# Performance work log

Hardware: AMD Instinct MI355X
Metric: run time of the kernel (lower is better)

## Reference

```python
import jax, jax.numpy as jnp
import numpy as np

B, S, D = 1, 4096, 512      # batch, seq, model dim
E, K, H = 64, 2, 256        # routed experts, top-k, expert hidden (moe_inter_dim)
HS = 2048                   # shared expert hidden = n_shared_experts * inter_dim
EPS = 1e-5                  # LayerNorm eps (torch default)


def setup_inputs() -> dict:
    key = jax.random.key(0)
    ks = jax.random.split(key, 16)
    n = lambda k, shp, s=0.02: jax.random.normal(k, shp, dtype=jnp.float32) * s
    return {
        "x": jax.random.normal(ks[0], (B, S, D), dtype=jnp.float32),
        # gate Linear(dim -> E)
        "Wg": n(ks[1], (E, D)), "bg": n(ks[2], (E,)),
        # per-expert LayerNorm affine
        "gamma": 1.0 + n(ks[3], (E, D)), "beta": n(ks[4], (E, D)),
        # per-expert SwiGLU: w1, w3: D->H ; w2: H->D
        "W1": n(ks[5], (E, D, H)), "b1": n(ks[6], (E, H)),
        "W3": n(ks[7], (E, D, H)), "b3": n(ks[8], (E, H)),
        "W2": n(ks[9], (E, H, D)), "b2": n(ks[10], (E, D)),
        # shared expert (same Expert structure, hidden HS)
        "gs": 1.0 + n(ks[11], (D,)), "bs": n(ks[11], (D,)),
        "Ws1": n(ks[12], (D, HS)), "bs1": n(ks[12], (HS,)),
        "Ws3": n(ks[13], (D, HS)), "bs3": n(ks[13], (HS,)),
        "Ws2": n(ks[14], (HS, D)), "bs2": n(ks[15], (D,)),
    }


def reference(x, Wg, bg, gamma, beta, W1, b1, W3, b3, W2, b2,
              gs, bs, Ws1, bs1, Ws3, bs3, Ws2, bs2):
    shape = x.shape
    xt = x.reshape(-1, D)                      # [T, D] tokens
    T = xt.shape[0]

    # ---- Gate (eval path: sigmoid scores, no load balancing / bias / groups) ----
    scores = jax.nn.sigmoid(xt @ Wg.T + bg)    # [T, E]
    w, idx = jax.lax.top_k(scores, K)          # [T, K]
    w = w / w.sum(-1, keepdims=True)           # sigmoid path normalization; route_scale = 1
    # dense combine weights: cw[t, e] = routing weight of token t on expert e (0 if not routed)
    cw = jnp.zeros((T, E), xt.dtype).at[jnp.arange(T)[:, None], idx].add(w)

    # ---- Shared LayerNorm statistics (affine folded per-expert below) ----
    mu = xt.mean(-1, keepdims=True)
    var = ((xt - mu) ** 2).mean(-1, keepdims=True)
    nx = (xt - mu) * jax.lax.rsqrt(var + EPS)  # [T, D], unit-affine normalized

    # Fold each expert's LN affine (gamma_e, beta_e) into its w1/w3:
    # (nx*g + b) @ W = nx @ (g[:,None]*W) + b @ W
    W1p = gamma[:, :, None] * W1
    b1p = b1 + jnp.einsum('ed,edh->eh', beta, W1)
    W3p = gamma[:, :, None] * W3
    b3p = b3 + jnp.einsum('ed,edh->eh', beta, W3)

    h1 = jnp.einsum('td,edh->eth', nx, W1p) + b1p[:, None, :]   # [E, T, H]
    h3 = jnp.einsum('td,edh->eth', nx, W3p) + b3p[:, None, :]
    h = jax.nn.silu(h1) * h3                                     # SwiGLU, [E, T, H]

    # Weighted combine: y[t] = sum_e cw[t,e] * (h[e,t] @ W2[e] + b2[e])
    hw = h * cw.T[:, :, None]                                    # [E, T, H]
    y = jnp.einsum('eth,ehd->td', hw, W2) + cw @ b2              # [T, D]

    # ---- Shared expert (applied to every token) ----
    nxs = nx * gs + bs
    hs = jax.nn.silu(nxs @ Ws1 + bs1) * (nxs @ Ws3 + bs3)        # [T, HS]
    z = hs @ Ws2 + bs2

    return (y + z).reshape(shape)
```

## Files before the change

### kernel.cpp

```cpp
#include <hip/hip_runtime.h>
#include <math.h>

typedef unsigned short u16;
typedef __attribute__((ext_vector_type(8))) short bf16x8;
typedef __attribute__((ext_vector_type(4))) float f32x4;

#define TT   4096
#define DM   512
#define NE   64
#define HE   256
#define HSH  2048
#define NSH  8
#define PADBASE 16384
#define MAXTILES 384
#define MAXRT    128

#define WAITV(N) asm volatile("s_waitcnt vmcnt(" #N ")" ::: "memory")
#define SBAR()   __builtin_amdgcn_s_barrier()
#define SCHEDB() __builtin_amdgcn_sched_barrier(0)

__device__ __forceinline__ float sig_(float z){ return 1.f/(1.f+__expf(-z)); }

__device__ __forceinline__ u16 f2bf(float x){
  unsigned int u = __builtin_bit_cast(unsigned int, x);
  u = (u + 0x7FFFu + ((u >> 16) & 1u)) >> 16;
  return (u16)u;
}

__device__ __forceinline__ f32x4 mfma16(bf16x8 a, bf16x8 b, f32x4 c){
  return __builtin_amdgcn_mfma_f32_16x16x32_bf16(a, b, c, 0, 0, 0);
}

__device__ __forceinline__ bf16x8 frd(const char* tile, int row, int csw){
  return *(const bf16x8*)(tile + row*64 + csw);
}

__device__ __forceinline__ void gl16(const void* g, void* l){
  __builtin_amdgcn_global_load_lds(
      (const __attribute__((address_space(1))) unsigned int*)g,
      (__attribute__((address_space(3))) unsigned int*)l, 16, 0, 0);
}

struct CvtJob {
  const float* in; const float* scale; const float* fvec;
  u16* out; float* fout; int K; int N; int base;
};
struct CvtJobs { CvtJob j[6]; };

__global__ __launch_bounds__(256) void k_cvt_all(CvtJobs jobs)
{
  const int bid = blockIdx.x;
  int ji = 0;
  #pragma unroll
  for (int i = 1; i < 6; i++) ji = (bid >= jobs.j[i].base) ? i : ji;
  const CvtJob J = jobs.j[ji];
  const int local = bid - J.base;
  const int nbx = J.K >> 6, nby = J.N >> 6;
  const int pm = nbx * nby;
  const int z = local / pm, rem = local - z*pm;
  const int bx = rem % nbx, by = rem / nbx;

  __shared__ u16 T[64][80];
  __shared__ float red[64][65];
  const int tid = threadIdx.x;
  const int k0 = bx*64, n0 = by*64;
  const float* ip = J.in + (size_t)z * J.K * J.N;
  const int r = tid>>2, cb = (tid&3)*16;
  const float sc = J.scale ? J.scale[(size_t)z*J.K + k0 + r] : 1.0f;
  const float fv = J.fvec  ? J.fvec [(size_t)z*J.K + k0 + r] : 0.0f;
  #pragma unroll
  for (int jj = 0; jj < 4; jj++){
    float4 v = *(const float4*)(ip + (size_t)(k0+r)*J.N + n0 + cb + jj*4);
    T[cb+jj*4+0][r] = f2bf(v.x*sc);
    T[cb+jj*4+1][r] = f2bf(v.y*sc);
    T[cb+jj*4+2][r] = f2bf(v.z*sc);
    T[cb+jj*4+3][r] = f2bf(v.w*sc);
    if (J.fout){
      red[cb+jj*4+0][r] = v.x*fv;
      red[cb+jj*4+1][r] = v.y*fv;
      red[cb+jj*4+2][r] = v.z*fv;
      red[cb+jj*4+3][r] = v.w*fv;
    }
  }
  __syncthreads();
  if (J.fout){
    const int c = tid & 63, rq = tid >> 6;
    float s = 0.f;
    #pragma unroll
    for (int rr = 0; rr < 16; rr++) s += red[c][rq*16 + rr];
    atomicAdd(J.fout + (size_t)z*J.N + n0 + c, s);
  }
  const int n = tid>>2, kb = (tid&3)*16;
  uint4 a = *(const uint4*)&T[n][kb];
  uint4 b = *(const uint4*)&T[n][kb+8];
  u16* op = J.out + (size_t)z*J.K*J.N;
  *(uint4*)(op + (size_t)(n0+n)*J.K + k0 + kb)     = a;
  *(uint4*)(op + (size_t)(n0+n)*J.K + k0 + kb + 8) = b;
}

__global__ __launch_bounds__(256) void k_ln_gate(
    const float* __restrict__ x, const float* __restrict__ Wg, const float* __restrict__ bg,
    u16* __restrict__ nxb, int* __restrict__ top_idx, float* __restrict__ top_w)
{
  __shared__ float xs[DM];
  __shared__ float sred[4], ssred[4];
  __shared__ float sc[NE];
  const int tid = threadIdx.x;
  const int t   = blockIdx.x;

  float2 v = reinterpret_cast<const float2*>(x + (size_t)t*DM)[tid];
  xs[2*tid]   = v.x;
  xs[2*tid+1] = v.y;
  float s  = v.x + v.y;
  float ss = v.x*v.x + v.y*v.y;
  #pragma unroll
  for (int o = 32; o > 0; o >>= 1){ s += __shfl_xor(s, o); ss += __shfl_xor(ss, o); }
  const int wid = tid >> 6, lane = tid & 63;
  if (lane == 0){ sred[wid] = s; ssred[wid] = ss; }
  __syncthreads();
  const float tot = sred[0]+sred[1]+sred[2]+sred[3];
  const float tss = ssred[0]+ssred[1]+ssred[2]+ssred[3];
  const float mu  = tot * (1.f/DM);
  const float var = tss * (1.f/DM) - mu*mu;
  const float rstd = rsqrtf(var + 1e-5f);
  unsigned int pk = (unsigned int)f2bf((v.x-mu)*rstd) | ((unsigned int)f2bf((v.y-mu)*rstd) << 16);
  *(unsigned int*)(nxb + (size_t)t*DM + 2*tid) = pk;

  const int e = tid >> 2, sub = tid & 3;
  const float4* wrow4 = reinterpret_cast<const float4*>(Wg + (size_t)e*DM);
  const float4* xs4   = reinterpret_cast<const float4*>(xs);
  float acc = 0.f;
  #pragma unroll 4
  for (int i = sub; i < DM/4; i += 4){
    const float4 w = wrow4[i]; const float4 xv = xs4[i];
    acc += xv.x*w.x + xv.y*w.y + xv.z*w.z + xv.w*w.w;
  }
  acc += __shfl_xor(acc, 1);
  acc += __shfl_xor(acc, 2);
  if (sub == 0) sc[e] = acc + bg[e];
  __syncthreads();

  if (tid < 64) {
    const float s0 = sc[tid];
    float m = s0; int mi = tid;
    #pragma unroll
    for (int o = 1; o < 64; o <<= 1){
      float om = __shfl_xor(m, o); int oi = __shfl_xor(mi, o);
      if (om > m || (om == m && oi < mi)) { m = om; mi = oi; }
    }
    float s1 = (tid == mi) ? -INFINITY : s0;
    float m2 = s1; int mi2 = tid;
    #pragma unroll
    for (int o = 1; o < 64; o <<= 1){
      float om = __shfl_xor(m2, o); int oi = __shfl_xor(mi2, o);
      if (om > m2 || (om == m2 && oi < mi2)) { m2 = om; mi2 = oi; }
    }
    if (tid == 0){
      const float w0 = sig_(m), w1 = sig_(m2);
      const float inv = 1.f/(w0+w1);
      top_idx[2*t]   = mi;
      top_idx[2*t+1] = mi2;
      top_w[2*t]     = w0*inv;
      top_w[2*t+1]   = w1*inv;
    }
  }
}

__global__ __launch_bounds__(256) void k_route(
    const int* __restrict__ top_idx, const float* __restrict__ top_w,
    int* __restrict__ bucket_tok, float* __restrict__ bucket_w,
    int* __restrict__ tiles, int* __restrict__ n_tiles)
{
  __shared__ int cnt[NE], base_[NE];
  __shared__ int nroute;
  const int tid = threadIdx.x;
  if (tid < NE) cnt[tid] = 0;
  __syncthreads();
  for (int p = tid; p < TT*2; p += 256) atomicAdd(&cnt[top_idx[p]], 1);
  __syncthreads();
  if (tid == 0){
    int run = 0, ntl = 0;
    for (int e = 0; e < NE; e++){
      base_[e] = run;
      const int c = cnt[e];
      for (int b = 0; b < c; b += 128){
        const int n = (c - b < 128) ? (c - b) : 128;
        tiles[ntl++] = (e << 17) | (((run + b) >> 7) << 8) | n;
      }
      run += ((c + 127) >> 7) << 7;
    }
    nroute = ntl;
    n_tiles[0] = ntl + NSH*(TT/128);
    n_tiles[1] = ntl;
  }
  __syncthreads();
  if (tid < NSH*(TT/128)){
    const int s = tid >> 5, t = tid & 31;
    const int b0 = PADBASE + s*TT + t*128;
    tiles[nroute + tid] = ((NE + s) << 17) | ((b0 >> 7) << 8) | 128;
  }
  if (tid < NE) cnt[tid] = 0;
  __syncthreads();
  for (int p = tid; p < TT*2; p += 256){
    const int e = top_idx[p];
    const int pos = base_[e] + atomicAdd(&cnt[e], 1);
    bucket_tok[pos] = p >> 1;
    bucket_w[pos]   = top_w[p];
  }
}

__global__ __launch_bounds__(512) void k_up(
    const u16* __restrict__ nxb,
    const u16* __restrict__ W1bT, const u16* __restrict__ W3bT,
    const u16* __restrict__ Ws1bT, const u16* __restrict__ Ws3bT,
    const float* __restrict__ b1, const float* __restrict__ b3,
    const float* __restrict__ bs1, const float* __restrict__ bs3,
    const float* __restrict__ b1f, const float* __restrict__ b3f,
    const int* __restrict__ bucket_tok, const float* __restrict__ bucket_w,
    const int* __restrict__ tiles, const int* __restrict__ n_tiles,
    u16* __restrict__ hrout, u16* __restrict__ hs)
{
  if ((int)blockIdx.x >= n_tiles[0]) return;
  const int info = tiles[blockIdx.x];
  const int e  = info >> 17;
  const int b0 = ((info >> 8) & 0x1FF) << 7;
  const int nt = info & 255;
  const bool sh = (e >= NE);
  const int y  = blockIdx.y;

  __shared__ __align__(16) char Ab[3][8192];
  __shared__ __align__(16) char B1b[3][8192];
  __shared__ __align__(16) char B3b[3][8192];
  __shared__ int   toks[128];
  __shared__ float tw[128];

  const int tid = threadIdx.x, wid = tid >> 6, lane = tid & 63;
  const int l15 = lane & 15, q = lane >> 4;

  if (tid < 128){
    int tk; float w;
    if (!sh){
      if (tid < nt){ tk = bucket_tok[b0+tid]; w = bucket_w[b0+tid]; }
      else         { tk = 0; w = 0.f; }
    } else {
      tk = ((b0 - PADBASE) & (TT-1)) + tid; w = 1.f;
    }
    toks[tid] = tk; tw[tid] = w;
  }
  __syncthreads();

  const u16* w1e = sh ? (Ws1bT + (size_t)(e-NE)*HE*DM) : (W1bT + (size_t)e*HE*DM);
  const u16* w3e = sh ? (Ws3bT + (size_t)(e-NE)*HE*DM) : (W3bT + (size_t)e*HE*DM);

  const int srow = lane >> 2;
  const int csrc = (((lane & 3) ^ ((lane >> 3) & 3))) * 8;
  const u16* asrc = nxb + (size_t)toks[wid*16 + srow]*DM + csrc;
  const u16* b1s  = w1e + (size_t)(y*128 + wid*16 + srow)*DM + csrc;
  const u16* b3s  = w3e + (size_t)(y*128 + wid*16 + srow)*DM + csrc;
  const int loff = wid*1024;

#define UP_STAGE(ph, k0) do{ \
    gl16(asrc + (k0), Ab[ph] + loff); \
    gl16(b1s  + (k0), B1b[ph] + loff); \
    gl16(b3s  + (k0), B3b[ph] + loff); \
  } while(0)

  const int wm = (wid & 1)*64, wn = (wid >> 1)*32;

  const float* ob1 = sh ? (bs1 + (size_t)(e-NE)*HE) : (b1 + (size_t)e*HE);
  const float* ob3 = sh ? (bs3 + (size_t)(e-NE)*HE) : (b3 + (size_t)e*HE);
  f32x4 acc1[4][2], acc3[4][2];
  #pragma unroll
  for (int fn = 0; fn < 2; fn++){
    const int h = y*128 + wn + fn*16 + l15;
    const float v1 = ob1[h] + b1f[(size_t)e*HE + h];
    const float v3 = ob3[h] + b3f[(size_t)e*HE + h];
    #pragma unroll
    for (int fm = 0; fm < 4; fm++){
      acc1[fm][fn] = (f32x4){v1,v1,v1,v1};
      acc3[fm][fn] = (f32x4){v3,v3,v3,v3};
    }
  }

  UP_STAGE(0, 0);
  UP_STAGE(1, 32);
  const int csw = (q ^ ((l15 >> 1) & 3)) * 16;

  for (int ks = 0; ks < DM/32; ks++){
    const int cur = ks % 3;
    if (ks + 2 < DM/32) UP_STAGE((ks+2)%3, (ks+2)*32);
    if (ks < DM/32 - 2)       WAITV(6);
    else if (ks == DM/32 - 2) WAITV(3);
    else                      WAITV(0);
    SBAR();
    __builtin_amdgcn_s_setprio(1);
    const char* A  = Ab[cur];
    const char* B1 = B1b[cur];
    const char* B3 = B3b[cur];
    bf16x8 fa[4];
    #pragma unroll
    for (int fm = 0; fm < 4; fm++) fa[fm] = frd(A, wm + fm*16 + l15, csw);
    #pragma unroll
    for (int fn = 0; fn < 2; fn++){
      bf16x8 fb1 = frd(B1, wn + fn*16 + l15, csw);
      bf16x8 fb3 = frd(B3, wn + fn*16 + l15, csw);
      #pragma unroll
      for (int fm = 0; fm < 4; fm++){
        acc1[fm][fn] = mfma16(fa[fm], fb1, acc1[fm][fn]);
        acc3[fm][fn] = mfma16(fa[fm], fb3, acc3[fm][fn]);
      }
    }
    __builtin_amdgcn_s_setprio(0);
    SCHEDB();
    SBAR();
  }
#undef UP_STAGE

  const int tbase = sh ? ((b0 - PADBASE) & (TT-1)) : 0;
  const int scol  = sh ? (e - NE)*HE : 0;
  #pragma unroll
  for (int fm = 0; fm < 4; fm++){
    #pragma unroll
    for (int fn = 0; fn < 2; fn++){
      const int hl = y*128 + wn + fn*16 + l15;
      #pragma unroll
      for (int r = 0; r < 4; r++){
        const int m = wm + fm*16 + 4*q + r;
        float v = 0.f;
        if (m < nt){
          const float a1 = acc1[fm][fn][r];
          const float a3 = acc3[fm][fn][r];
          v = a1 * sig_(a1) * a3 * tw[m];
        }
        if (sh) hs[(size_t)(tbase+m)*HSH + scol + hl] = f2bf(v);
        else    hrout[(size_t)(b0+m)*HE + hl] = f2bf(v);
      }
    }
  }
}

__global__ __launch_bounds__(256) void k_down_shared(
    const u16* __restrict__ hs, const u16* __restrict__ Ws2bT,
    const float* __restrict__ bs2, float* __restrict__ out)
{
  __shared__ __align__(16) char Ab[3][4096];
  __shared__ __align__(16) char Bb[3][8192];

  const int tid = threadIdx.x, wid = tid >> 6, lane = tid & 63;
  const int l15 = lane & 15, q = lane >> 4;
  const int t0 = blockIdx.x*64, d0 = blockIdx.y*128;

  const int srow = tid >> 2;
  const int csrc = (((tid & 3) ^ ((tid >> 3) & 3))) * 8;
  const u16* asrc  = hs    + (size_t)(t0 + srow)*HSH + csrc;
  const u16* bsrc0 = Ws2bT + (size_t)(d0 + srow)*HSH + csrc;
  const u16* bsrc1 = Ws2bT + (size_t)(d0 + 64 + srow)*HSH + csrc;
  const int loff = wid*1024;

#define DS_STAGE(ph, k0) do{ \
    gl16(asrc  + (k0), Ab[ph] + loff); \
    gl16(bsrc0 + (k0), Bb[ph] + loff); \
    gl16(bsrc1 + (k0), Bb[ph] + 4096 + loff); \
  } while(0)

  const int wm = (wid & 1)*32, wn = (wid >> 1)*64;

  f32x4 acc[2][4];
  #pragma unroll
  for (int fm = 0; fm < 2; fm++)
    #pragma unroll
    for (int fn = 0; fn < 4; fn++) acc[fm][fn] = (f32x4){0.f,0.f,0.f,0.f};

  DS_STAGE(0, 0);
  DS_STAGE(1, 32);
  const int csw = (q ^ ((l15 >> 1) & 3)) * 16;

  for (int ks = 0; ks < HSH/32; ks++){
    const int cur = ks % 3;
    if (ks + 2 < HSH/32) DS_STAGE((ks+2)%3, (ks+2)*32);
    if (ks < HSH/32 - 2)       WAITV(6);
    else if (ks == HSH/32 - 2) WAITV(3);
    else                       WAITV(0);
    SBAR();
    __builtin_amdgcn_s_setprio(1);
    const char* A = Ab[cur];
    const char* B = Bb[cur];
    bf16x8 fa[2];
    #pragma unroll
    for (int fm = 0; fm < 2; fm++) fa[fm] = frd(A, wm + fm*16 + l15, csw);
    #pragma unroll
    for (int fn = 0; fn < 4; fn++){
      bf16x8 fb = frd(B, wn + fn*16 + l15, csw);
      #pragma unroll
      for (int fm = 0; fm < 2; fm++)
        acc[fm][fn] = mfma16(fa[fm], fb, acc[fm][fn]);
    }
    __builtin_amdgcn_s_setprio(0);
    SCHEDB();
    SBAR();
  }
#undef DS_STAGE

  #pragma unroll
  for (int fm = 0; fm < 2; fm++){
    #pragma unroll
    for (int fn = 0; fn < 4; fn++){
      const int d = d0 + wn + fn*16 + l15;
      const float bv = bs2[d];
      #pragma unroll
      for (int r = 0; r < 4; r++){
        const int t = t0 + wm + fm*16 + 4*q + r;
        out[(size_t)t*DM + d] = acc[fm][fn][r] + bv;
      }
    }
  }
}

__global__ __launch_bounds__(512) void k_down_routed(
    const u16* __restrict__ hrout, const u16* __restrict__ W2bT,
    const float* __restrict__ b2,
    const int* __restrict__ bucket_tok, const float* __restrict__ bucket_w,
    const int* __restrict__ tiles, const int* __restrict__ n_tiles,
    float* __restrict__ out)
{
  if ((int)blockIdx.x >= n_tiles[1]) return;
  const int info = tiles[blockIdx.x];
  const int e  = info >> 17;
  const int b0 = ((info >> 8) & 0x1FF) << 7;
  const int nt = info & 255;
  const int d0 = blockIdx.y * 256;

  __shared__ __align__(16) char Ab[3][8192];
  __shared__ __align__(16) char Bb[3][16384];
  __shared__ int   toks[128];
  __shared__ float tw[128];

  const int tid = threadIdx.x, wid = tid >> 6, lane = tid & 63;
  const int l15 = lane & 15, q = lane >> 4;

  if (tid < 128){
    if (tid < nt){ toks[tid] = bucket_tok[b0+tid]; tw[tid] = bucket_w[b0+tid]; }
    else         { toks[tid] = 0; tw[tid] = 0.f; }
  }
  __syncthreads();

  const u16* w2e = W2bT + (size_t)e*DM*HE;
  const int srow = tid >> 2;
  const int csrc = (((tid & 3) ^ ((tid >> 3) & 3))) * 8;
  const u16* asrc  = hrout + (size_t)(b0 + srow)*HE + csrc;
  const u16* bsrc0 = w2e + (size_t)(d0 + srow)*HE + csrc;
  const u16* bsrc1 = w2e + (size_t)(d0 + 128 + srow)*HE + csrc;
  const int loff = wid*1024;

#define DR_STAGE(ph, k0) do{ \
    gl16(asrc  + (k0), Ab[ph] + loff); \
    gl16(bsrc0 + (k0), Bb[ph] + loff); \
    gl16(bsrc1 + (k0), Bb[ph] + 8192 + loff); \
  } while(0)

  const int wm = (wid & 1)*64, wn = (wid >> 1)*64;

  f32x4 acc[4][4];
  #pragma unroll
  for (int fm = 0; fm < 4; fm++)
    #pragma unroll
    for (int fn = 0; fn < 4; fn++) acc[fm][fn] = (f32x4){0.f,0.f,0.f,0.f};

  DR_STAGE(0, 0);
  DR_STAGE(1, 32);
  const int csw = (q ^ ((l15 >> 1) & 3)) * 16;

  for (int ks = 0; ks < HE/32; ks++){
    const int cur = ks % 3;
    if (ks + 2 < HE/32) DR_STAGE((ks+2)%3, (ks+2)*32);
    if (ks < HE/32 - 2)       WAITV(6);
    else if (ks == HE/32 - 2) WAITV(3);
    else                      WAITV(0);
    SBAR();
    __builtin_amdgcn_s_setprio(1);
    const char* A = Ab[cur];
    const char* B = Bb[cur];
    bf16x8 fa[4];
    #pragma unroll
    for (int fm = 0; fm < 4; fm++) fa[fm] = frd(A, wm + fm*16 + l15, csw);
    #pragma unroll
    for (int fn = 0; fn < 4; fn++){
      bf16x8 fb = frd(B, wn + fn*16 + l15, csw);
      #pragma unroll
      for (int fm = 0; fm < 4; fm++)
        acc[fm][fn] = mfma16(fa[fm], fb, acc[fm][fn]);
    }
    __builtin_amdgcn_s_setprio(0);
    SCHEDB();
    SBAR();
  }
#undef DR_STAGE

  #pragma unroll
  for (int fm = 0; fm < 4; fm++){
    #pragma unroll
    for (int fn = 0; fn < 4; fn++){
      const int d = d0 + wn + fn*16 + l15;
      #pragma unroll
      for (int r = 0; r < 4; r++){
        const int m = wm + fm*16 + 4*q + r;
        if (m < nt)
          atomicAdd(out + (size_t)toks[m]*DM + d, acc[fm][fn][r] + tw[m]*b2[(size_t)e*DM + d]);
      }
    }
  }
}

extern "C" void kernel_launch(void* const* d_in, const int* in_sizes, int n_in,
                              void* d_out, int out_size, void* d_ws, size_t ws_size,
                              hipStream_t stream)
{
  (void)in_sizes; (void)n_in; (void)ws_size; (void)out_size;
  const float* x     = (const float*)d_in[0];
  const float* Wg    = (const float*)d_in[1];
  const float* bg    = (const float*)d_in[2];
  const float* gamma = (const float*)d_in[3];
  const float* beta  = (const float*)d_in[4];
  const float* W1    = (const float*)d_in[5];
  const float* b1    = (const float*)d_in[6];
  const float* W3    = (const float*)d_in[7];
  const float* b3    = (const float*)d_in[8];
  const float* W2    = (const float*)d_in[9];
  const float* b2    = (const float*)d_in[10];
  const float* gs    = (const float*)d_in[11];
  const float* bs    = (const float*)d_in[12];
  const float* Ws1   = (const float*)d_in[13];
  const float* bs1   = (const float*)d_in[14];
  const float* Ws3   = (const float*)d_in[15];
  const float* bs3   = (const float*)d_in[16];
  const float* Ws2   = (const float*)d_in[17];
  const float* bs2   = (const float*)d_in[18];
  float* out = (float*)d_out;

  char* ws = (char*)d_ws;
  size_t off = 0;
  auto alloc = [&](size_t bytes) -> char* {
    char* p = ws + off;
    off += (bytes + 255) & ~(size_t)255;
    return p;
  };
  u16*   nxb        = (u16*)  alloc((size_t)TT*DM*2);
  int*   top_idx    = (int*)  alloc((size_t)TT*2*4);
  float* top_w      = (float*)alloc((size_t)TT*2*4);
  int*   bucket_tok = (int*)  alloc((size_t)PADBASE*4);
  float* bucket_w   = (float*)alloc((size_t)PADBASE*4);
  int*   tiles      = (int*)  alloc(MAXTILES*4);
  int*   n_tiles    = (int*)  alloc(64);
  u16*   hrout      = (u16*)  alloc((size_t)PADBASE*HE*2);
  u16*   hs         = (u16*)  alloc((size_t)TT*HSH*2);
  u16*   W1bT       = (u16*)  alloc((size_t)NE*HE*DM*2);
  u16*   W3bT       = (u16*)  alloc((size_t)NE*HE*DM*2);
  u16*   W2bT       = (u16*)  alloc((size_t)NE*DM*HE*2);
  u16*   Ws1bT      = (u16*)  alloc((size_t)HSH*DM*2);
  u16*   Ws3bT      = (u16*)  alloc((size_t)HSH*DM*2);
  u16*   Ws2bT      = (u16*)  alloc((size_t)DM*HSH*2);
  float* b1f        = (float*)alloc((size_t)(NE*HE + HSH)*4);
  float* b3f        = (float*)alloc((size_t)(NE*HE + HSH)*4);

  hipMemsetAsync(b1f, 0, (size_t)(NE*HE + HSH)*4, stream);
  hipMemsetAsync(b3f, 0, (size_t)(NE*HE + HSH)*4, stream);
  CvtJobs jobs;
  jobs.j[0] = { W1,  gamma, beta, W1bT,  b1f,          DM,  HE,  0    };
  jobs.j[1] = { W3,  gamma, beta, W3bT,  b3f,          DM,  HE,  2048 };
  jobs.j[2] = { W2,  nullptr, nullptr, W2bT, nullptr,  HE,  DM,  4096 };
  jobs.j[3] = { Ws1, gs, bs, Ws1bT, b1f + NE*HE,       DM,  HSH, 6144 };
  jobs.j[4] = { Ws3, gs, bs, Ws3bT, b3f + NE*HE,       DM,  HSH, 6400 };
  jobs.j[5] = { Ws2, nullptr, nullptr, Ws2bT, nullptr, HSH, DM,  6656 };
  k_cvt_all<<<dim3(6912), 256, 0, stream>>>(jobs);

  k_ln_gate<<<dim3(TT), 256, 0, stream>>>(x, Wg, bg, nxb, top_idx, top_w);
  k_route<<<dim3(1), 256, 0, stream>>>(top_idx, top_w, bucket_tok, bucket_w, tiles, n_tiles);

  k_up<<<dim3(MAXTILES, 2), 512, 0, stream>>>(nxb, W1bT, W3bT, Ws1bT, Ws3bT,
                                              b1, b3, bs1, bs3, b1f, b3f,
                                              bucket_tok, bucket_w, tiles, n_tiles, hrout, hs);
  k_down_shared<<<dim3(TT/64, DM/128), 256, 0, stream>>>(hs, Ws2bT, bs2, out);
  k_down_routed<<<dim3(MAXRT, 2), 512, 0, stream>>>(hrout, W2bT, b2,
                                                    bucket_tok, bucket_w, tiles, n_tiles, out);
}
```

Baseline: 204.9 us.

## Merge weight conversion with LN/gate and fuse shared and routed down kernels

```diff
diff --git a/kernel.cpp b/kernel.cpp
--- a/kernel.cpp
+++ b/kernel.cpp
@@ -2,6 +2,7 @@
 #include <math.h>
 
 typedef unsigned short u16;
+typedef unsigned int u32;
 typedef __attribute__((ext_vector_type(8))) short bf16x8;
 typedef __attribute__((ext_vector_type(4))) float f32x4;
 
@@ -22,7 +23,7 @@
 __device__ __forceinline__ float sig_(float z){ return 1.f/(1.f+__expf(-z)); }
 
 __device__ __forceinline__ u16 f2bf(float x){
-  unsigned int u = __builtin_bit_cast(unsigned int, x);
+  u32 u = __builtin_bit_cast(u32, x);
   u = (u + 0x7FFFu + ((u >> 16) & 1u)) >> 16;
   return (u16)u;
 }
@@ -47,66 +48,66 @@
 };
 struct CvtJobs { CvtJob j[6]; };
 
-__global__ __launch_bounds__(256) void k_cvt_all(CvtJobs jobs)
+__global__ __launch_bounds__(256) void k_pre(
+    CvtJobs jobs, int ln_base,
+    const float* __restrict__ x, const float* __restrict__ Wg,
+    const float* __restrict__ bg,
+    u16* __restrict__ nxb, int* __restrict__ top_idx, float* __restrict__ top_w)
 {
   const int bid = blockIdx.x;
-  int ji = 0;
-  #pragma unroll
-  for (int i = 1; i < 6; i++) ji = (bid >= jobs.j[i].base) ? i : ji;
-  const CvtJob J = jobs.j[ji];
-  const int local = bid - J.base;
-  const int nbx = J.K >> 6, nby = J.N >> 6;
-  const int pm = nbx * nby;
-  const int z = local / pm, rem = local - z*pm;
-  const int bx = rem % nbx, by = rem / nbx;
-
-  __shared__ u16 T[64][80];
-  __shared__ float red[64][65];
   const int tid = threadIdx.x;
-  const int k0 = bx*64, n0 = by*64;
-  const float* ip = J.in + (size_t)z * J.K * J.N;
-  const int r = tid>>2, cb = (tid&3)*16;
-  const float sc = J.scale ? J.scale[(size_t)z*J.K + k0 + r] : 1.0f;
-  const float fv = J.fvec  ? J.fvec [(size_t)z*J.K + k0 + r] : 0.0f;
-  #pragma unroll
-  for (int jj = 0; jj < 4; jj++){
-    float4 v = *(const float4*)(ip + (size_t)(k0+r)*J.N + n0 + cb + jj*4);
-    T[cb+jj*4+0][r] = f2bf(v.x*sc);
-    T[cb+jj*4+1][r] = f2bf(v.y*sc);
-    T[cb+jj*4+2][r] = f2bf(v.z*sc);
-    T[cb+jj*4+3][r] = f2bf(v.w*sc);
-    if (J.fout){
-      red[cb+jj*4+0][r] = v.x*fv;
-      red[cb+jj*4+1][r] = v.y*fv;
-      red[cb+jj*4+2][r] = v.z*fv;
-      red[cb+jj*4+3][r] = v.w*fv;
-    }
-  }
-  __syncthreads();
-  if (J.fout){
-    const int c = tid & 63, rq = tid >> 6;
-    float s = 0.f;
-    #pragma unroll
-    for (int rr = 0; rr < 16; rr++) s += red[c][rq*16 + rr];
-    atomicAdd(J.fout + (size_t)z*J.N + n0 + c, s);
-  }
-  const int n = tid>>2, kb = (tid&3)*16;
-  uint4 a = *(const uint4*)&T[n][kb];
-  uint4 b = *(const uint4*)&T[n][kb+8];
-  u16* op = J.out + (size_t)z*J.K*J.N;
-  *(uint4*)(op + (size_t)(n0+n)*J.K + k0 + kb)     = a;
-  *(uint4*)(op + (size_t)(n0+n)*J.K + k0 + kb + 8) = b;
-}
-
-__global__ __launch_bounds__(256) void k_ln_gate(
-    const float* __restrict__ x, const float* __restrict__ Wg, const float* __restrict__ bg,
-    u16* __restrict__ nxb, int* __restrict__ top_idx, float* __restrict__ top_w)
-{
+
+  if (bid < ln_base){
+    int ji = 0;
+    #pragma unroll
+    for (int i = 1; i < 6; i++) ji = (bid >= jobs.j[i].base) ? i : ji;
+    const CvtJob J = jobs.j[ji];
+    const int local = bid - J.base;
+    const int nbk = J.K >> 6;
+    const int nbn = J.N >> 8;
+    const int pm = nbk * nbn;
+    const int z = local / pm, rem = local - z*pm;
+    const int kt = rem % nbk, ntile = rem / nbk;
+    const int k0 = kt*64;
+    const int n  = ntile*256 + tid;
+
+    const float* src = J.in + (size_t)z*J.K*J.N + (size_t)k0*J.N + n;
+    const float* scp = J.scale ? (J.scale + (size_t)z*J.K + k0) : nullptr;
+    const float* fvp = J.fvec  ? (J.fvec  + (size_t)z*J.K + k0) : nullptr;
+    u16* dst = J.out + (size_t)z*J.K*J.N + (size_t)n*J.K + k0;
+
+    float fsum = 0.f;
+    for (int kk = 0; kk < 8; kk++){
+      float v[8];
+      #pragma unroll
+      for (int j = 0; j < 8; j++) v[j] = src[(size_t)(kk*8 + j)*J.N];
+      u16 b[8];
+      if (scp){
+        #pragma unroll
+        for (int j = 0; j < 8; j++) b[j] = f2bf(v[j]*scp[kk*8 + j]);
+      } else {
+        #pragma unroll
+        for (int j = 0; j < 8; j++) b[j] = f2bf(v[j]);
+      }
+      if (fvp){
+        #pragma unroll
+        for (int j = 0; j < 8; j++) fsum += v[j]*fvp[kk*8 + j];
+      }
+      uint4 pk;
+      pk.x = (u32)b[0] | ((u32)b[1] << 16);
+      pk.y = (u32)b[2] | ((u32)b[3] << 16);
+      pk.z = (u32)b[4] | ((u32)b[5] << 16);
+      pk.w = (u32)b[6] | ((u32)b[7] << 16);
+      *(uint4*)(dst + kk*8) = pk;
+    }
+    if (J.fout) atomicAdd(J.fout + (size_t)z*J.N + n, fsum);
+    return;
+  }
+
   __shared__ float xs[DM];
   __shared__ float sred[4], ssred[4];
   __shared__ float sc[NE];
-  const int tid = threadIdx.x;
-  const int t   = blockIdx.x;
+  const int t = bid - ln_base;
 
   float2 v = reinterpret_cast<const float2*>(x + (size_t)t*DM)[tid];
   xs[2*tid]   = v.x;
@@ -123,8 +124,8 @@
   const float mu  = tot * (1.f/DM);
   const float var = tss * (1.f/DM) - mu*mu;
   const float rstd = rsqrtf(var + 1e-5f);
-  unsigned int pk = (unsigned int)f2bf((v.x-mu)*rstd) | ((unsigned int)f2bf((v.y-mu)*rstd) << 16);
-  *(unsigned int*)(nxb + (size_t)t*DM + 2*tid) = pk;
+  u32 pk = (u32)f2bf((v.x-mu)*rstd) | ((u32)f2bf((v.y-mu)*rstd) << 16);
+  *(u32*)(nxb + (size_t)t*DM + 2*tid) = pk;
 
   const int e = tid >> 2, sub = tid & 3;
   const float4* wrow4 = reinterpret_cast<const float4*>(Wg + (size_t)e*DM);
@@ -339,104 +340,104 @@
   }
 }
 
-__global__ __launch_bounds__(256) void k_down_shared(
+__global__ __launch_bounds__(512) void k_down(
     const u16* __restrict__ hs, const u16* __restrict__ Ws2bT,
-    const float* __restrict__ bs2, float* __restrict__ out)
-{
-  __shared__ __align__(16) char Ab[3][4096];
-  __shared__ __align__(16) char Bb[3][8192];
-
-  const int tid = threadIdx.x, wid = tid >> 6, lane = tid & 63;
-  const int l15 = lane & 15, q = lane >> 4;
-  const int t0 = blockIdx.x*64, d0 = blockIdx.y*128;
-
-  const int srow = tid >> 2;
-  const int csrc = (((tid & 3) ^ ((tid >> 3) & 3))) * 8;
-  const u16* asrc  = hs    + (size_t)(t0 + srow)*HSH + csrc;
-  const u16* bsrc0 = Ws2bT + (size_t)(d0 + srow)*HSH + csrc;
-  const u16* bsrc1 = Ws2bT + (size_t)(d0 + 64 + srow)*HSH + csrc;
-  const int loff = wid*1024;
-
-#define DS_STAGE(ph, k0) do{ \
-    gl16(asrc  + (k0), Ab[ph] + loff); \
-    gl16(bsrc0 + (k0), Bb[ph] + loff); \
-    gl16(bsrc1 + (k0), Bb[ph] + 4096 + loff); \
-  } while(0)
-
-  const int wm = (wid & 1)*32, wn = (wid >> 1)*64;
-
-  f32x4 acc[2][4];
-  #pragma unroll
-  for (int fm = 0; fm < 2; fm++)
-    #pragma unroll
-    for (int fn = 0; fn < 4; fn++) acc[fm][fn] = (f32x4){0.f,0.f,0.f,0.f};
-
-  DS_STAGE(0, 0);
-  DS_STAGE(1, 32);
-  const int csw = (q ^ ((l15 >> 1) & 3)) * 16;
-
-  for (int ks = 0; ks < HSH/32; ks++){
-    const int cur = ks % 3;
-    if (ks + 2 < HSH/32) DS_STAGE((ks+2)%3, (ks+2)*32);
-    if (ks < HSH/32 - 2)       WAITV(6);
-    else if (ks == HSH/32 - 2) WAITV(3);
-    else                       WAITV(0);
-    SBAR();
-    __builtin_amdgcn_s_setprio(1);
-    const char* A = Ab[cur];
-    const char* B = Bb[cur];
-    bf16x8 fa[2];
-    #pragma unroll
-    for (int fm = 0; fm < 2; fm++) fa[fm] = frd(A, wm + fm*16 + l15, csw);
-    #pragma unroll
-    for (int fn = 0; fn < 4; fn++){
-      bf16x8 fb = frd(B, wn + fn*16 + l15, csw);
-      #pragma unroll
-      for (int fm = 0; fm < 2; fm++)
-        acc[fm][fn] = mfma16(fa[fm], fb, acc[fm][fn]);
-    }
-    __builtin_amdgcn_s_setprio(0);
-    SCHEDB();
-    SBAR();
-  }
-#undef DS_STAGE
-
-  #pragma unroll
-  for (int fm = 0; fm < 2; fm++){
-    #pragma unroll
-    for (int fn = 0; fn < 4; fn++){
-      const int d = d0 + wn + fn*16 + l15;
-      const float bv = bs2[d];
-      #pragma unroll
-      for (int r = 0; r < 4; r++){
-        const int t = t0 + wm + fm*16 + 4*q + r;
-        out[(size_t)t*DM + d] = acc[fm][fn][r] + bv;
-      }
-    }
-  }
-}
-
-__global__ __launch_bounds__(512) void k_down_routed(
+    const float* __restrict__ bs2,
     const u16* __restrict__ hrout, const u16* __restrict__ W2bT,
     const float* __restrict__ b2,
     const int* __restrict__ bucket_tok, const float* __restrict__ bucket_w,
     const int* __restrict__ tiles, const int* __restrict__ n_tiles,
     float* __restrict__ out)
 {
-  if ((int)blockIdx.x >= n_tiles[1]) return;
-  const int info = tiles[blockIdx.x];
+  __shared__ __align__(16) char LDS[73728];
+  __shared__ int   toks[128];
+  __shared__ float tw[128];
+
+  const int tid = threadIdx.x, wid = tid >> 6, lane = tid & 63;
+  const int l15 = lane & 15, q = lane >> 4;
+  const int csw  = (q ^ ((l15 >> 1) & 3)) * 16;
+  const int srow = tid >> 2;
+  const int csrc = ((tid & 3) ^ ((tid >> 3) & 3)) * 8;
+  const int loff = wid*1024;
+
+  if ((int)blockIdx.x < 128){
+    const int t0 = (blockIdx.x >> 2) * 128;
+    const int d0 = (blockIdx.x & 3) * 128;
+    char* Ab = LDS;
+    char* Bb = LDS + 24576;
+
+    const u16* asrc = hs    + (size_t)(t0 + srow)*HSH + csrc;
+    const u16* bsrc = Ws2bT + (size_t)(d0 + srow)*HSH + csrc;
+
+#define DS_STAGE(ph, k0) do{ \
+    gl16(asrc + (k0), Ab + (ph)*8192 + loff); \
+    gl16(bsrc + (k0), Bb + (ph)*8192 + loff); \
+  } while(0)
+
+    const int wm = (wid & 1)*64, wn = (wid >> 1)*32;
+
+    f32x4 acc[4][2];
+    #pragma unroll
+    for (int fm = 0; fm < 4; fm++)
+      #pragma unroll
+      for (int fn = 0; fn < 2; fn++) acc[fm][fn] = (f32x4){0.f,0.f,0.f,0.f};
+
+    DS_STAGE(0, 0);
+    DS_STAGE(1, 32);
+
+    for (int ks = 0; ks < HSH/32; ks++){
+      const int cur = ks % 3;
+      if (ks + 2 < HSH/32) DS_STAGE((ks+2)%3, (ks+2)*32);
+      if (ks < HSH/32 - 2)       WAITV(4);
+      else if (ks == HSH/32 - 2) WAITV(2);
+      else                       WAITV(0);
+      SBAR();
+      __builtin_amdgcn_s_setprio(1);
+      const char* A = Ab + cur*8192;
+      const char* B = Bb + cur*8192;
+      bf16x8 fa[4];
+      #pragma unroll
+      for (int fm = 0; fm < 4; fm++) fa[fm] = frd(A, wm + fm*16 + l15, csw);
+      #pragma unroll
+      for (int fn = 0; fn < 2; fn++){
+        bf16x8 fb = frd(B, wn + fn*16 + l15, csw);
+        #pragma unroll
+        for (int fm = 0; fm < 4; fm++)
+          acc[fm][fn] = mfma16(fa[fm], fb, acc[fm][fn]);
+      }
+      __builtin_amdgcn_s_setprio(0);
+      SCHEDB();
+      SBAR();
+    }
+#undef DS_STAGE
+
+    #pragma unroll
+    for (int fm = 0; fm < 4; fm++){
+      #pragma unroll
+      for (int fn = 0; fn < 2; fn++){
+        const int d = d0 + wn + fn*16 + l15;
+        const float bv = bs2[d];
+        #pragma unroll
+        for (int r = 0; r < 4; r++){
+          const int t = t0 + wm + fm*16 + 4*q + r;
+          atomicAdd(out + (size_t)t*DM + d, acc[fm][fn][r] + bv);
+        }
+      }
+    }
+    return;
+  }
+
+  const int rb = (int)blockIdx.x - 128;
+  const int ti = rb >> 1;
+  if (ti >= n_tiles[1]) return;
+  const int info = tiles[ti];
   const int e  = info >> 17;
   const int b0 = ((info >> 8) & 0x1FF) << 7;
   const int nt = info & 255;
-  const int d0 = blockIdx.y * 256;
-
-  __shared__ __align__(16) char Ab[3][8192];
-  __shared__ __align__(16) char Bb[3][16384];
-  __shared__ int   toks[128];
-  __shared__ float tw[128];
-
-  const int tid = threadIdx.x, wid = tid >> 6, lane = tid & 63;
-  const int l15 = lane & 15, q = lane >> 4;
+  const int d0 = (rb & 1) * 256;
+
+  char* Ab = LDS;
+  char* Bb = LDS + 24576;
 
   if (tid < 128){
     if (tid < nt){ toks[tid] = bucket_tok[b0+tid]; tw[tid] = bucket_w[b0+tid]; }
@@ -445,17 +446,14 @@
   __syncthreads();
 
   const u16* w2e = W2bT + (size_t)e*DM*HE;
-  const int srow = tid >> 2;
-  const int csrc = (((tid & 3) ^ ((tid >> 3) & 3))) * 8;
   const u16* asrc  = hrout + (size_t)(b0 + srow)*HE + csrc;
   const u16* bsrc0 = w2e + (size_t)(d0 + srow)*HE + csrc;
   const u16* bsrc1 = w2e + (size_t)(d0 + 128 + srow)*HE + csrc;
-  const int loff = wid*1024;
 
 #define DR_STAGE(ph, k0) do{ \
-    gl16(asrc  + (k0), Ab[ph] + loff); \
-    gl16(bsrc0 + (k0), Bb[ph] + loff); \
-    gl16(bsrc1 + (k0), Bb[ph] + 8192 + loff); \
+    gl16(asrc  + (k0), Ab + (ph)*8192  + loff); \
+    gl16(bsrc0 + (k0), Bb + (ph)*16384 + loff); \
+    gl16(bsrc1 + (k0), Bb + (ph)*16384 + 8192 + loff); \
   } while(0)
 
   const int wm = (wid & 1)*64, wn = (wid >> 1)*64;
@@ -468,7 +466,6 @@
 
   DR_STAGE(0, 0);
   DR_STAGE(1, 32);
-  const int csw = (q ^ ((l15 >> 1) & 3)) * 16;
 
   for (int ks = 0; ks < HE/32; ks++){
     const int cur = ks % 3;
@@ -478,8 +475,8 @@
     else                      WAITV(0);
     SBAR();
     __builtin_amdgcn_s_setprio(1);
-    const char* A = Ab[cur];
-    const char* B = Bb[cur];
+    const char* A = Ab + cur*8192;
+    const char* B = Bb + cur*16384;
     bf16x8 fa[4];
     #pragma unroll
     for (int fm = 0; fm < 4; fm++) fa[fm] = frd(A, wm + fm*16 + l15, csw);
@@ -515,7 +512,7 @@
                               void* d_out, int out_size, void* d_ws, size_t ws_size,
                               hipStream_t stream)
 {
-  (void)in_sizes; (void)n_in; (void)ws_size; (void)out_size;
+  (void)in_sizes; (void)n_in; (void)ws_size;
   const float* x     = (const float*)d_in[0];
   const float* Wg    = (const float*)d_in[1];
   const float* bg    = (const float*)d_in[2];
@@ -564,22 +561,24 @@
 
   hipMemsetAsync(b1f, 0, (size_t)(NE*HE + HSH)*4, stream);
   hipMemsetAsync(b3f, 0, (size_t)(NE*HE + HSH)*4, stream);
+  hipMemsetAsync(out, 0, (size_t)out_size*sizeof(float), stream);
+
   CvtJobs jobs;
-  jobs.j[0] = { W1,  gamma, beta, W1bT,  b1f,          DM,  HE,  0    };
-  jobs.j[1] = { W3,  gamma, beta, W3bT,  b3f,          DM,  HE,  2048 };
-  jobs.j[2] = { W2,  nullptr, nullptr, W2bT, nullptr,  HE,  DM,  4096 };
-  jobs.j[3] = { Ws1, gs, bs, Ws1bT, b1f + NE*HE,       DM,  HSH, 6144 };
-  jobs.j[4] = { Ws3, gs, bs, Ws3bT, b3f + NE*HE,       DM,  HSH, 6400 };
-  jobs.j[5] = { Ws2, nullptr, nullptr, Ws2bT, nullptr, HSH, DM,  6656 };
-  k_cvt_all<<<dim3(6912), 256, 0, stream>>>(jobs);
-
-  k_ln_gate<<<dim3(TT), 256, 0, stream>>>(x, Wg, bg, nxb, top_idx, top_w);
+  jobs.j[0] = { W1,  gamma,   beta,    W1bT,  b1f,          DM,  HE,  0    };
+  jobs.j[1] = { W3,  gamma,   beta,    W3bT,  b3f,          DM,  HE,  512  };
+  jobs.j[2] = { W2,  nullptr, nullptr, W2bT,  nullptr,      HE,  DM,  1024 };
+  jobs.j[3] = { Ws1, gs,      bs,      Ws1bT, b1f + NE*HE,  DM,  HSH, 1536 };
+  jobs.j[4] = { Ws3, gs,      bs,      Ws3bT, b3f + NE*HE,  DM,  HSH, 1600 };
+  jobs.j[5] = { Ws2, nullptr, nullptr, Ws2bT, nullptr,      HSH, DM,  1664 };
+  const int ln_base = 1728;
+  k_pre<<<dim3(ln_base + TT), 256, 0, stream>>>(jobs, ln_base,
+                                                x, Wg, bg, nxb, top_idx, top_w);
+
   k_route<<<dim3(1), 256, 0, stream>>>(top_idx, top_w, bucket_tok, bucket_w, tiles, n_tiles);
 
   k_up<<<dim3(MAXTILES, 2), 512, 0, stream>>>(nxb, W1bT, W3bT, Ws1bT, Ws3bT,
                                               b1, b3, bs1, bs3, b1f, b3f,
                                               bucket_tok, bucket_w, tiles, n_tiles, hrout, hs);
-  k_down_shared<<<dim3(TT/64, DM/128), 256, 0, stream>>>(hs, Ws2bT, bs2, out);
-  k_down_routed<<<dim3(MAXRT, 2), 512, 0, stream>>>(hrout, W2bT, b2,
-                                                    bucket_tok, bucket_w, tiles, n_tiles, out);
-}
+  k_down<<<dim3(384), 512, 0, stream>>>(hs, Ws2bT, bs2, hrout, W2bT, b2,
+                                        bucket_tok, bucket_w, tiles, n_tiles, out);
+}
```

Measured after the change: 221.8 us. +8.3%, slower.
